# Kernel tuning notes

Hardware: AMD Instinct MI355X
Metric: run time of the kernel (lower is better)

Reference implementation:

```python
import jax, jax.numpy as jnp
import numpy as np

D_MODEL = 1024
NUM_HEADS = 16
HEAD_DIM = D_MODEL // NUM_HEADS
D_FF = 4096
BATCH = 4
SEQ = 2048
LN_EPS = 1e-6
NEG_INF = -1e10


def setup_inputs() -> dict:
    key = jax.random.key(0)
    ks = jax.random.split(key, 8)
    def lin_init(k, fan_in, fan_out):
        # flax default: lecun_normal kernel, zeros bias
        w = jax.random.normal(k, (fan_in, fan_out), jnp.float32) / np.sqrt(fan_in)
        b = jnp.zeros((fan_out,), jnp.float32)
        return w, b
    x = jax.random.normal(ks[0], (BATCH, SEQ, D_MODEL), jnp.float32)
    w_qkv, b_qkv = lin_init(ks[1], D_MODEL, 3 * D_MODEL)
    w_out, b_out = lin_init(ks[2], D_MODEL, D_MODEL)
    w_fc1, b_fc1 = lin_init(ks[3], D_MODEL, D_FF)
    w_fc2, b_fc2 = lin_init(ks[4], D_FF, D_MODEL)
    ln1_scale = jnp.ones((D_MODEL,), jnp.float32)
    ln1_bias = jnp.zeros((D_MODEL,), jnp.float32)
    ln2_scale = jnp.ones((D_MODEL,), jnp.float32)
    ln2_bias = jnp.zeros((D_MODEL,), jnp.float32)
    return {
        'x': x,
        'w_qkv': w_qkv, 'b_qkv': b_qkv,
        'w_out': w_out, 'b_out': b_out,
        'w_fc1': w_fc1, 'b_fc1': b_fc1,
        'w_fc2': w_fc2, 'b_fc2': b_fc2,
        'ln1_scale': ln1_scale, 'ln1_bias': ln1_bias,
        'ln2_scale': ln2_scale, 'ln2_bias': ln2_bias,
    }


def _layernorm(x, scale, bias):
    mu = jnp.mean(x, axis=-1, keepdims=True)
    var = jnp.mean(jnp.square(x - mu), axis=-1, keepdims=True)
    return (x - mu) * jax.lax.rsqrt(var + LN_EPS) * scale + bias


def _attention(x, w_qkv, b_qkv, w_out, b_out):
    B, S, _ = x.shape
    qkv = x @ w_qkv + b_qkv                      # [B,S,3*D]
    qkv = qkv.reshape(B, S, 3, NUM_HEADS, HEAD_DIM)
    q, k, v = qkv[:, :, 0], qkv[:, :, 1], qkv[:, :, 2]   # [B,S,H,D]
    q = q.transpose(0, 2, 1, 3)                  # [B,H,S,D]
    k = k.transpose(0, 2, 1, 3)
    v = v.transpose(0, 2, 1, 3)
    scores = jnp.einsum('bhqd,bhkd->bhqk', q, k) / np.sqrt(HEAD_DIM)
    causal = jnp.tril(jnp.ones((S, S), bool))[None, None]
    scores = jnp.where(causal, scores, NEG_INF)
    attn = jax.nn.softmax(scores, axis=-1)
    out = jnp.einsum('bhqk,bhkd->bhqd', attn, v)  # [B,H,S,D]
    out = out.transpose(0, 2, 1, 3).reshape(B, S, D_MODEL)
    return out @ w_out + b_out


def _mlp(x, w_fc1, b_fc1, w_fc2, b_fc2):
    h = jax.nn.gelu(x @ w_fc1 + b_fc1)  # approximate (tanh) gelu, matching nnx.gelu default
    return h @ w_fc2 + b_fc2


def reference(x, w_qkv, b_qkv, w_out, b_out, w_fc1, b_fc1, w_fc2, b_fc2,
              ln1_scale, ln1_bias, ln2_scale, ln2_bias):
    x = x + _attention(_layernorm(x, ln1_scale, ln1_bias), w_qkv, b_qkv, w_out, b_out)
    x = x + _mlp(_layernorm(x, ln2_scale, ln2_bias), w_fc1, b_fc1, w_fc2, b_fc2)
    return x
```

## Files before the change

kernel.cpp:

```cpp
#include <hip/hip_runtime.h>

typedef unsigned short u16;
typedef unsigned int u32;
typedef __bf16 bf16x8 __attribute__((ext_vector_type(8)));
typedef float f32x4 __attribute__((ext_vector_type(4)));

constexpr int SEQ = 2048;

__device__ __forceinline__ float bf2f(u16 u) {
    u32 x = ((u32)u) << 16;
    return __builtin_bit_cast(float, x);
}
__device__ __forceinline__ u16 f2bf(float f) {
    u32 u = __builtin_bit_cast(u32, f);
    u32 r = u + 0x7fffu + ((u >> 16) & 1u);
    return (u16)(r >> 16);
}
__device__ __forceinline__ u32 cvt_pk_bf16(float a, float b) {
    u32 d;
    asm("v_cvt_pk_bf16_f32 %0, %1, %2" : "=v"(d) : "v"(a), "v"(b));
    return d;
}
__device__ __forceinline__ bf16x8 ld_frag(const u16* p) {
    uint4 u = *(const uint4*)p;
    return __builtin_bit_cast(bf16x8, u);
}
__device__ __forceinline__ float gelu_f(float x) {
    float u = 0.7978845608028654f * (x + 0.044715f * x * x * x);
    float e = exp2f(u * 2.885390081777927f);
    float t = 1.f - 2.f / (1.f + e);
    return 0.5f * x * (1.f + t);
}
__device__ __forceinline__ bool probe_f32(const u32* p) { return (p[0] & 0xFFFFu) == 0u; }

__device__ __forceinline__ void load_lds16(const u16* g, u16* l) {
    __builtin_amdgcn_global_load_lds(
        (const __attribute__((address_space(1))) void*)g,
        (__attribute__((address_space(3))) void*)l, 16, 0, 0);
}

__device__ __forceinline__ void xcd_map(int& bx, int& by) {
    const int gx = gridDim.x;
    const int n = gx * gridDim.y;
    const int orig = blockIdx.y * gx + blockIdx.x;
    const int id = (orig & 7) * (n >> 3) + (orig >> 3);
    bx = id % gx;
    by = id / gx;
}

__global__ __launch_bounds__(256) void convert_to_bf16(const void* __restrict__ in, long long off,
                                                       u16* __restrict__ out, int n,
                                                       const u32* __restrict__ probe) {
    const bool f32 = probe_f32(probe);
    int i = (blockIdx.x * 256 + threadIdx.x) * 4;
    if (i >= n) return;
    if (f32) {
        const float4 v = *(const float4*)((const float*)in + off + i);
        uint2 o;
        o.x = (u32)f2bf(v.x) | ((u32)f2bf(v.y) << 16);
        o.y = (u32)f2bf(v.z) | ((u32)f2bf(v.w) << 16);
        *(uint2*)(out + i) = o;
    } else {
        *(uint2*)(out + i) = *(const uint2*)((const u16*)in + off + i);
    }
}

__global__ __launch_bounds__(256) void transpose_any(const void* __restrict__ in,
                                                     u16* __restrict__ out,
                                                     int K, int N, const u32* __restrict__ probe) {
    const bool f32 = probe_f32(probe);
    __shared__ u16 tile[32][33];
    int tx = threadIdx.x & 31, ty = threadIdx.x >> 5;
    int k0 = blockIdx.y * 32, n0 = blockIdx.x * 32;
    for (int i = 0; i < 32; i += 8) {
        size_t idx = (size_t)(k0 + ty + i) * N + n0 + tx;
        tile[ty + i][tx] = f32 ? f2bf(((const float*)in)[idx]) : ((const u16*)in)[idx];
    }
    __syncthreads();
    for (int i = 0; i < 32; i += 8)
        out[(size_t)(n0 + ty + i) * K + k0 + tx] = tile[tx][ty + i];
}

__global__ __launch_bounds__(256) void fused_cvt_ln(const void* __restrict__ xraw, long long off,
                                                    const u16* __restrict__ sc,
                                                    const u16* __restrict__ bi,
                                                    u16* __restrict__ xbf,
                                                    u16* __restrict__ xn,
                                                    const u32* __restrict__ probe) {
    const bool f32 = probe_f32(probe);
    int row = blockIdx.x;
    int tid = threadIdx.x;
    float v[4];
    if (f32) {
        const float4 q = *(const float4*)((const float*)xraw + off + (size_t)row * 1024 + tid * 4);
        v[0] = q.x; v[1] = q.y; v[2] = q.z; v[3] = q.w;
    } else {
        uint2 u = *(const uint2*)((const u16*)xraw + off + (size_t)row * 1024 + tid * 4);
        v[0] = bf2f((u16)(u.x & 0xffffu)); v[1] = bf2f((u16)(u.x >> 16));
        v[2] = bf2f((u16)(u.y & 0xffffu)); v[3] = bf2f((u16)(u.y >> 16));
    }
    {
        uint2 c;
        c.x = (u32)f2bf(v[0]) | ((u32)f2bf(v[1]) << 16);
        c.y = (u32)f2bf(v[2]) | ((u32)f2bf(v[3]) << 16);
        *(uint2*)(xbf + (size_t)row * 1024 + tid * 4) = c;
    }
    float s1 = 0.f, s2 = 0.f;
    for (int i = 0; i < 4; i++) { s1 += v[i]; s2 += v[i] * v[i]; }
    for (int off2 = 32; off2 >= 1; off2 >>= 1) {
        s1 += __shfl_xor(s1, off2, 64);
        s2 += __shfl_xor(s2, off2, 64);
    }
    __shared__ float red[8];
    int wave = tid >> 6, lane = tid & 63;
    if (lane == 0) { red[wave] = s1; red[4 + wave] = s2; }
    __syncthreads();
    s1 = red[0] + red[1] + red[2] + red[3];
    s2 = red[4] + red[5] + red[6] + red[7];
    float mean = s1 * (1.f / 1024.f);
    float var = s2 * (1.f / 1024.f) - mean * mean;
    float rstd = rsqrtf(var + 1e-6f);
    int c = tid * 4;
    float y0 = (v[0] - mean) * rstd * bf2f(sc[c + 0]) + bf2f(bi[c + 0]);
    float y1 = (v[1] - mean) * rstd * bf2f(sc[c + 1]) + bf2f(bi[c + 1]);
    float y2 = (v[2] - mean) * rstd * bf2f(sc[c + 2]) + bf2f(bi[c + 2]);
    float y3 = (v[3] - mean) * rstd * bf2f(sc[c + 3]) + bf2f(bi[c + 3]);
    uint2 ov;
    ov.x = (u32)f2bf(y0) | ((u32)f2bf(y1) << 16);
    ov.y = (u32)f2bf(y2) | ((u32)f2bf(y3) << 16);
    *(uint2*)(xn + (size_t)row * 1024 + tid * 4) = ov;
}

__global__ __launch_bounds__(256) void layernorm_k(const u16* __restrict__ x,
                                                   const u16* __restrict__ sc,
                                                   const u16* __restrict__ bi,
                                                   u16* __restrict__ out) {
    int row = blockIdx.x;
    int tid = threadIdx.x;
    const u16* xr = x + (size_t)row * 1024;
    uint2 u = *(const uint2*)(xr + tid * 4);
    float v[4];
    v[0] = bf2f((u16)(u.x & 0xffffu));
    v[1] = bf2f((u16)(u.x >> 16));
    v[2] = bf2f((u16)(u.y & 0xffffu));
    v[3] = bf2f((u16)(u.y >> 16));
    float s1 = 0.f, s2 = 0.f;
    for (int i = 0; i < 4; i++) { s1 += v[i]; s2 += v[i] * v[i]; }
    for (int off = 32; off >= 1; off >>= 1) {
        s1 += __shfl_xor(s1, off, 64);
        s2 += __shfl_xor(s2, off, 64);
    }
    __shared__ float red[8];
    int wave = tid >> 6, lane = tid & 63;
    if (lane == 0) { red[wave] = s1; red[4 + wave] = s2; }
    __syncthreads();
    s1 = red[0] + red[1] + red[2] + red[3];
    s2 = red[4] + red[5] + red[6] + red[7];
    float mean = s1 * (1.f / 1024.f);
    float var = s2 * (1.f / 1024.f) - mean * mean;
    float rstd = rsqrtf(var + 1e-6f);
    u32 o0, o1;
    {
        int c = tid * 4;
        float y0 = (v[0] - mean) * rstd * bf2f(sc[c + 0]) + bf2f(bi[c + 0]);
        float y1 = (v[1] - mean) * rstd * bf2f(sc[c + 1]) + bf2f(bi[c + 1]);
        float y2 = (v[2] - mean) * rstd * bf2f(sc[c + 2]) + bf2f(bi[c + 2]);
        float y3 = (v[3] - mean) * rstd * bf2f(sc[c + 3]) + bf2f(bi[c + 3]);
        o0 = (u32)f2bf(y0) | ((u32)f2bf(y1) << 16);
        o1 = (u32)f2bf(y2) | ((u32)f2bf(y3) << 16);
    }
    uint2 ov; ov.x = o0; ov.y = o1;
    *(uint2*)(out + (size_t)row * 1024 + tid * 4) = ov;
}

__device__ __forceinline__ void gemm_core(const u16* __restrict__ A, const u16* __restrict__ Bt,
                                          int K, int bm, int bn,
                                          u16* lA, u16* lB, f32x4 acc[4][4]) {
    const int tid = threadIdx.x, lane = tid & 63, wave = tid >> 6;
    const int wr = (wave >> 1) * 64, wc = (wave & 1) * 64;
    const int g = lane >> 4, l15 = lane & 15;
    const int srow = wave * 32 + (lane >> 3);
    const int gslot = (lane & 7) ^ (lane >> 3);
    const u16* gA = A + (size_t)(bm + srow) * K + gslot * 8;
    const u16* gB = Bt + (size_t)(bn + srow) * K + gslot * 8;
    const int sw = (l15 & 7);
    const int nt = K >> 6;

    {
        u16* dA = lA + wave * 2048;
        u16* dB = lB + wave * 2048;
#pragma unroll
        for (int q = 0; q < 4; q++) {
            load_lds16(gA + q * 8 * K, dA + q * 512);
            load_lds16(gB + q * 8 * K, dB + q * 512);
        }
    }

    for (int t = 0; t < nt; t++) {
        const int cur = (t & 1) * 8192;
        __syncthreads();
        if (t + 1 < nt) {
            const int nxt = ((t + 1) & 1) * 8192;
            const int kk = (t + 1) * 64;
            u16* dA = lA + nxt + wave * 2048;
            u16* dB = lB + nxt + wave * 2048;
#pragma unroll
            for (int q = 0; q < 4; q++) {
                load_lds16(gA + kk + q * 8 * K, dA + q * 512);
                load_lds16(gB + kk + q * 8 * K, dB + q * 512);
            }
        }
        const u16* cA = lA + cur;
        const u16* cB = lB + cur;
#pragma unroll
        for (int kh = 0; kh < 2; kh++) {
            bf16x8 af[4], bfr[4];
#pragma unroll
            for (int i = 0; i < 4; i++)
                af[i] = ld_frag(cA + (wr + i * 16 + l15) * 64 + (((kh * 4 + g) ^ sw) * 8));
#pragma unroll
            for (int j = 0; j < 4; j++)
                bfr[j] = ld_frag(cB + (wc + j * 16 + l15) * 64 + (((kh * 4 + g) ^ sw) * 8));
#pragma unroll
            for (int i = 0; i < 4; i++)
#pragma unroll
                for (int j = 0; j < 4; j++)
                    acc[i][j] = __builtin_amdgcn_mfma_f32_16x16x32_bf16(bfr[j], af[i], acc[i][j], 0, 0, 0);
        }
    }
}

__global__ __launch_bounds__(256) void gemm_bt(const u16* __restrict__ A,
                                               const u16* __restrict__ Bt,
                                               const u16* __restrict__ bias,
                                               const u16* __restrict__ res,
                                               void* __restrict__ out,
                                               int M, int N, int K, int epi,
                                               long long ooff, const u32* __restrict__ probe) {
    __shared__ __align__(16) u16 lA[2 * 128 * 64];
    __shared__ __align__(16) u16 lB[2 * 128 * 64];
    const int tid = threadIdx.x, lane = tid & 63, wave = tid >> 6;
    const int wr = (wave >> 1) * 64, wc = (wave & 1) * 64;
    const int g = lane >> 4, l15 = lane & 15;
    int bxi, byi;
    xcd_map(bxi, byi);
    const int bm = byi * 128, bn = bxi * 128;

    f32x4 acc[4][4];
    f32x4 zero = {0.f, 0.f, 0.f, 0.f};
    for (int i = 0; i < 4; i++)
        for (int j = 0; j < 4; j++) acc[i][j] = zero;

    gemm_core(A, Bt, K, bm, bn, lA, lB, acc);

    const bool of32 = (epi == 3) && probe_f32(probe);
    for (int j = 0; j < 4; j++) {
        const int gn0 = bn + wc + j * 16 + g * 4;
        const uint2 bv2 = *(const uint2*)(bias + gn0);
        const float b0 = bf2f((u16)(bv2.x & 0xffffu)), b1 = bf2f((u16)(bv2.x >> 16));
        const float b2 = bf2f((u16)(bv2.y & 0xffffu)), b3 = bf2f((u16)(bv2.y >> 16));
        for (int i = 0; i < 4; i++) {
            const int gm = bm + wr + i * 16 + l15;
            float v0 = acc[i][j][0] + b0, v1 = acc[i][j][1] + b1;
            float v2 = acc[i][j][2] + b2, v3 = acc[i][j][3] + b3;
            if (epi == 1 || epi == 3) {
                const uint2 rv = *(const uint2*)(res + (size_t)gm * N + gn0);
                v0 += bf2f((u16)(rv.x & 0xffffu)); v1 += bf2f((u16)(rv.x >> 16));
                v2 += bf2f((u16)(rv.y & 0xffffu)); v3 += bf2f((u16)(rv.y >> 16));
            } else if (epi == 2) {
                v0 = gelu_f(v0); v1 = gelu_f(v1); v2 = gelu_f(v2); v3 = gelu_f(v3);
            }
            if (epi == 3) {
                if (of32) {
                    float4 o = {v0, v1, v2, v3};
                    *(float4*)((float*)out + ooff + (size_t)gm * N + gn0) = o;
                } else {
                    uint2 o;
                    o.x = cvt_pk_bf16(v0, v1); o.y = cvt_pk_bf16(v2, v3);
                    *(uint2*)((u16*)out + ooff + (size_t)gm * N + gn0) = o;
                }
            } else {
                uint2 o;
                o.x = cvt_pk_bf16(v0, v1); o.y = cvt_pk_bf16(v2, v3);
                *(uint2*)((u16*)out + (size_t)gm * N + gn0) = o;
            }
        }
    }
}

__global__ __launch_bounds__(256) void gemm_qkv(const u16* __restrict__ A,
                                                const u16* __restrict__ Bt,
                                                const u16* __restrict__ bias,
                                                u16* __restrict__ Qg,
                                                u16* __restrict__ Kg,
                                                u16* __restrict__ VTg,
                                                int K) {
    __shared__ __align__(16) u16 lA[2 * 128 * 64];
    __shared__ __align__(16) u16 lB[2 * 128 * 64];
    const int tid = threadIdx.x, lane = tid & 63, wave = tid >> 6;
    const int wr = (wave >> 1) * 64, wc = (wave & 1) * 64;
    const int g = lane >> 4, l15 = lane & 15;
    int bxi, byi;
    xcd_map(bxi, byi);
    const int bm = byi * 128, bn = bxi * 128;
    const float QSCALE = 0.18033688011112042f;

    f32x4 acc[4][4];
    f32x4 zero = {0.f, 0.f, 0.f, 0.f};
    for (int i = 0; i < 4; i++)
        for (int j = 0; j < 4; j++) acc[i][j] = zero;

    gemm_core(A, Bt, K, bm, bn, lA, lB, acc);

    for (int j = 0; j < 4; j++) {
        const int gn0 = bn + wc + j * 16 + g * 4;
        const int which = gn0 >> 10;
        const int hh = (gn0 >> 6) & 15, d0 = gn0 & 63;
        const uint2 bv2 = *(const uint2*)(bias + gn0);
        const float b0 = bf2f((u16)(bv2.x & 0xffffu)), b1 = bf2f((u16)(bv2.x >> 16));
        const float b2 = bf2f((u16)(bv2.y & 0xffffu)), b3 = bf2f((u16)(bv2.y >> 16));
        for (int i = 0; i < 4; i++) {
            const int s0 = bm + wr + i * 16 + l15;
            const int b = s0 >> 11, srel = s0 & 2047;
            const int bh = b * 16 + hh;
            const float v0 = acc[i][j][0] + b0, v1 = acc[i][j][1] + b1;
            const float v2 = acc[i][j][2] + b2, v3 = acc[i][j][3] + b3;
            if (which == 0) {
                uint2 o;
                o.x = cvt_pk_bf16(v0 * QSCALE, v1 * QSCALE);
                o.y = cvt_pk_bf16(v2 * QSCALE, v3 * QSCALE);
                *(uint2*)(Qg + ((size_t)bh * SEQ + srel) * 64 + d0) = o;
            } else if (which == 1) {
                uint2 o;
                o.x = cvt_pk_bf16(v0, v1); o.y = cvt_pk_bf16(v2, v3);
                *(uint2*)(Kg + ((size_t)bh * SEQ + srel) * 64 + d0) = o;
            } else {
                VTg[((size_t)bh * 64 + d0 + 0) * SEQ + srel] = f2bf(v0);
                VTg[((size_t)bh * 64 + d0 + 1) * SEQ + srel] = f2bf(v1);
                VTg[((size_t)bh * 64 + d0 + 2) * SEQ + srel] = f2bf(v2);
                VTg[((size_t)bh * 64 + d0 + 3) * SEQ + srel] = f2bf(v3);
            }
        }
    }
}

__device__ __forceinline__ void stage_kv(const u16* Kbh, const u16* Vbh, int kv0,
                                         u16* bK, u16* bV, int lane, int wave) {
    const int r = lane >> 3;
    const int gs = ((lane & 7) ^ r) * 8;
#pragma unroll
    for (int q = 0; q < 2; q++) {
        const int row = q * 32 + wave * 8 + r;
        load_lds16(Kbh + (size_t)(kv0 + row) * 64 + gs, bK + q * 2048 + wave * 512 + lane * 8);
        load_lds16(Vbh + (size_t)row * SEQ + kv0 + gs, bV + q * 2048 + wave * 512 + lane * 8);
    }
}

__global__ __launch_bounds__(256) void flash_attn6(const u16* __restrict__ Qg,
                                                   const u16* __restrict__ Kg,
                                                   const u16* __restrict__ VTg,
                                                   u16* __restrict__ attn) {
    __shared__ __align__(16) u16 lK[2][64 * 64];
    __shared__ __align__(16) u16 lVt[2][64 * 64];
    __shared__ __align__(16) u16 lP[4 * 32 * 72];

    int bxi, byi;
    xcd_map(bxi, byi);
    const int bh = byi;
    const int tid = threadIdx.x, lane = tid & 63, wave = tid >> 6;
    const int g = lane >> 4, l15 = lane & 15;
    const float MASKV = -3.0e4f;

    const u16* Qbh = Qg + (size_t)bh * SEQ * 64;
    const u16* Kbh = Kg + (size_t)bh * SEQ * 64;
    const u16* Vbh = VTg + (size_t)bh * 64 * SEQ;
    u16* myP = lP + wave * 32 * 72;
    const int b = bh >> 4, h = bh & 15;
    const f32x4 zero = {0.f, 0.f, 0.f, 0.f};
    const int sw = (l15 & 7);

    for (int ph = 0; ph < 2; ph++) {
        const int ti = ph ? bxi : (15 - bxi);
        const int q0 = ti * 128;
        const int qw = q0 + wave * 32;
        const int nfull = q0 >> 6;
        const int nt = nfull + 2;

        bf16x8 qf[2][2];
#pragma unroll
        for (int mi = 0; mi < 2; mi++)
#pragma unroll
            for (int kh = 0; kh < 2; kh++)
                qf[mi][kh] = ld_frag(Qbh + (size_t)(qw + mi * 16 + l15) * 64 + kh * 32 + g * 8);

        float l_[2] = {0.f, 0.f};
        f32x4 o[2][4];
        for (int mi = 0; mi < 2; mi++)
            for (int nj = 0; nj < 4; nj++) o[mi][nj] = zero;

        __syncthreads();
        stage_kv(Kbh, Vbh, 0, lK[0], lVt[0], lane, wave);

        for (int t = 0; t < nt; t++) {
            __syncthreads();
            if (t + 1 < nt)
                stage_kv(Kbh, Vbh, (t + 1) * 64, lK[(t + 1) & 1], lVt[(t + 1) & 1], lane, wave);
            const u16* bK = lK[t & 1];
            const u16* bV = lVt[t & 1];
            const bool diag = (t >= nfull);
            const int kv0 = t * 64;

            f32x4 sc[4][2];
#pragma unroll
            for (int ki = 0; ki < 4; ki++)
                for (int mi = 0; mi < 2; mi++) sc[ki][mi] = zero;
#pragma unroll
            for (int kh = 0; kh < 2; kh++) {
                bf16x8 kf[4];
#pragma unroll
                for (int ki = 0; ki < 4; ki++)
                    kf[ki] = ld_frag(bK + (ki * 16 + l15) * 64 + (((kh * 4 + g) ^ sw) * 8));
#pragma unroll
                for (int ki = 0; ki < 4; ki++)
#pragma unroll
                    for (int mi = 0; mi < 2; mi++)
                        sc[ki][mi] = __builtin_amdgcn_mfma_f32_16x16x32_bf16(kf[ki], qf[mi][kh], sc[ki][mi], 0, 0, 0);
            }

#pragma unroll
            for (int mi = 0; mi < 2; mi++) {
                const int qrow = qw + mi * 16 + l15;
                u16* pr = myP + (mi * 16 + l15) * 72 + g * 4;
                float lacc = 0.f;
#pragma unroll
                for (int ki = 0; ki < 4; ki++) {
                    const int kvb = kv0 + ki * 16 + g * 4;
                    float v0 = sc[ki][mi][0], v1 = sc[ki][mi][1];
                    float v2 = sc[ki][mi][2], v3 = sc[ki][mi][3];
                    if (diag) {
                        if (kvb + 0 > qrow) v0 = MASKV;
                        if (kvb + 1 > qrow) v1 = MASKV;
                        if (kvb + 2 > qrow) v2 = MASKV;
                        if (kvb + 3 > qrow) v3 = MASKV;
                    }
                    const float e0 = exp2f(v0), e1 = exp2f(v1);
                    const float e2 = exp2f(v2), e3 = exp2f(v3);
                    lacc += (e0 + e1) + (e2 + e3);
                    uint2 pw;
                    pw.x = cvt_pk_bf16(e0, e1);
                    pw.y = cvt_pk_bf16(e2, e3);
                    *(uint2*)(pr + ki * 16) = pw;
                }
                l_[mi] += lacc;
            }

#pragma unroll
            for (int ks = 0; ks < 2; ks++) {
                bf16x8 pa[2], vb[4];
#pragma unroll
                for (int mi = 0; mi < 2; mi++)
                    pa[mi] = ld_frag(myP + (mi * 16 + l15) * 72 + ks * 32 + g * 8);
#pragma unroll
                for (int nj = 0; nj < 4; nj++)
                    vb[nj] = ld_frag(bV + (nj * 16 + l15) * 64 + (((ks * 4 + g) ^ sw) * 8));
#pragma unroll
                for (int mi = 0; mi < 2; mi++)
#pragma unroll
                    for (int nj = 0; nj < 4; nj++)
                        o[mi][nj] = __builtin_amdgcn_mfma_f32_16x16x32_bf16(pa[mi], vb[nj], o[mi][nj], 0, 0, 0);
            }
        }

#pragma unroll
        for (int mi = 0; mi < 2; mi++) {
            float ls = l_[mi];
            ls += __shfl_xor(ls, 16, 64);
            ls += __shfl_xor(ls, 32, 64);
#pragma unroll
            for (int r = 0; r < 4; r++) {
                const float inv = 1.f / __shfl(ls, g * 4 + r, 64);
                const int row = qw + mi * 16 + g * 4 + r;
                const size_t orow = ((size_t)b * SEQ + row) * 1024 + h * 64;
                for (int nj = 0; nj < 4; nj++)
                    attn[orow + nj * 16 + l15] = f2bf(o[mi][nj][r] * inv);
            }
        }
    }
}

extern "C" void kernel_launch(void* const* d_in, const int* in_sizes, int n_in,
                              void* d_out, int out_size, void* d_ws, size_t ws_size,
                              hipStream_t stream) {
    const u32* probe = (const u32*)d_in[9];
    char* ws = (char*)d_ws;
    const size_t MB = 1048576;
    auto T = [&](size_t mb) { return (u16*)(ws + mb * MB); };
    auto conv = [&](const void* src, long long off, u16* dst, int n) {
        convert_to_bf16<<<(n / 4 + 255) / 256, 256, 0, stream>>>(src, off, dst, n, probe);
    };

    if (ws_size >= 160 * MB) {
        u16* xn1 = T(0), *Qg = T(16), *Kg = T(32), *VTg = T(48), *hbuf = T(0);
        u16* attn = T(64), *xn2 = T(64), *xbf = T(80), *resid1 = T(96);
        u16* wTq = T(128), *wTo = T(134), *wT1 = T(136), *wT2 = T(144), *vecs = T(152);
        u16 *bqkvC = vecs, *boutC = vecs + 3072, *bfc1C = vecs + 4096, *bfc2C = vecs + 8192;
        u16 *ln1sC = vecs + 9216, *ln1bC = vecs + 10240, *ln2sC = vecs + 11264, *ln2bC = vecs + 12288;
        conv(d_in[2], 0, bqkvC, 3072); conv(d_in[4], 0, boutC, 1024);
        conv(d_in[6], 0, bfc1C, 4096); conv(d_in[8], 0, bfc2C, 1024);
        conv(d_in[9], 0, ln1sC, 1024); conv(d_in[10], 0, ln1bC, 1024);
        conv(d_in[11], 0, ln2sC, 1024); conv(d_in[12], 0, ln2bC, 1024);
        transpose_any<<<dim3(96, 32), 256, 0, stream>>>(d_in[1], wTq, 1024, 3072, probe);
        transpose_any<<<dim3(32, 32), 256, 0, stream>>>(d_in[3], wTo, 1024, 1024, probe);
        transpose_any<<<dim3(128, 32), 256, 0, stream>>>(d_in[5], wT1, 1024, 4096, probe);
        transpose_any<<<dim3(32, 128), 256, 0, stream>>>(d_in[7], wT2, 4096, 1024, probe);
        fused_cvt_ln<<<8192, 256, 0, stream>>>(d_in[0], 0, ln1sC, ln1bC, xbf, xn1, probe);
        gemm_qkv<<<dim3(24, 64), 256, 0, stream>>>(xn1, wTq, bqkvC, Qg, Kg, VTg, 1024);
        flash_attn6<<<dim3(8, 64), 256, 0, stream>>>(Qg, Kg, VTg, attn);
        gemm_bt<<<dim3(8, 64), 256, 0, stream>>>(attn, wTo, boutC, xbf, resid1, 8192, 1024, 1024, 1, 0, probe);
        layernorm_k<<<8192, 256, 0, stream>>>(resid1, ln2sC, ln2bC, xn2);
        gemm_bt<<<dim3(32, 64), 256, 0, stream>>>(xn2, wT1, bfc1C, nullptr, hbuf, 8192, 4096, 1024, 2, 0, probe);
        gemm_bt<<<dim3(8, 64), 256, 0, stream>>>(hbuf, wT2, bfc2C, resid1, d_out, 8192, 1024, 4096, 3, 0, probe);
    } else {
        u16* vecs = T(0);
        u16 *bqkvC = vecs, *boutC = vecs + 3072, *bfc1C = vecs + 4096, *bfc2C = vecs + 8192;
        u16 *ln1sC = vecs + 9216, *ln1bC = vecs + 10240, *ln2sC = vecs + 11264, *ln2bC = vecs + 12288;
        u16* wTq = T(1), *wTo = T(7), *wT1 = T(9), *wT2 = T(17);
        u16* xbf = T(25), *xn = T(29), *Qg = T(33), *Kg = T(37), *VTg = T(41);
        u16* attn_b = T(45), *resid_b = T(49), *h_b = T(53);
        conv(d_in[2], 0, bqkvC, 3072); conv(d_in[4], 0, boutC, 1024);
        conv(d_in[6], 0, bfc1C, 4096); conv(d_in[8], 0, bfc2C, 1024);
        conv(d_in[9], 0, ln1sC, 1024); conv(d_in[10], 0, ln1bC, 1024);
        conv(d_in[11], 0, ln2sC, 1024); conv(d_in[12], 0, ln2bC, 1024);
        transpose_any<<<dim3(96, 32), 256, 0, stream>>>(d_in[1], wTq, 1024, 3072, probe);
        transpose_any<<<dim3(32, 32), 256, 0, stream>>>(d_in[3], wTo, 1024, 1024, probe);
        transpose_any<<<dim3(128, 32), 256, 0, stream>>>(d_in[5], wT1, 1024, 4096, probe);
        transpose_any<<<dim3(32, 128), 256, 0, stream>>>(d_in[7], wT2, 4096, 1024, probe);
        for (int b = 0; b < 4; b++) {
            const long long ro = (long long)b * 2048 * 1024;
            fused_cvt_ln<<<2048, 256, 0, stream>>>(d_in[0], ro, ln1sC, ln1bC, xbf, xn, probe);
            gemm_qkv<<<dim3(24, 16), 256, 0, stream>>>(xn, wTq, bqkvC, Qg, Kg, VTg, 1024);
            flash_attn6<<<dim3(8, 16), 256, 0, stream>>>(Qg, Kg, VTg, attn_b);
            gemm_bt<<<dim3(8, 16), 256, 0, stream>>>(attn_b, wTo, boutC, xbf, resid_b, 2048, 1024, 1024, 1, 0, probe);
            layernorm_k<<<2048, 256, 0, stream>>>(resid_b, ln2sC, ln2bC, xn);
            for (int c = 0; c < 2; c++) {
                u16* xnc = xn + (size_t)c * 1024 * 1024;
                u16* resc = resid_b + (size_t)c * 1024 * 1024;
                gemm_bt<<<dim3(32, 8), 256, 0, stream>>>(xnc, wT1, bfc1C, nullptr, h_b, 1024, 4096, 1024, 2, 0, probe);
                gemm_bt<<<dim3(8, 8), 256, 0, stream>>>(h_b, wT2, bfc2C, resc, d_out, 1024, 1024, 4096, 3, ro + (long long)c * 1048576, probe);
            }
        }
    }
}
```

Measured before the change: 539.5 us.

## Replace double-buffered GEMM LDS pipeline with single buffer and optional XCD remap

The shared GEMM core drops its double-buffered LDS prefetch in favour of a single 128x64 buffer per operand, with a barrier before and after each tile load. This halves LDS use per block, which may allow more resident blocks per CU, but it removes the overlap of global loads with MFMA work. A remap flag also disables the XCD block remapping for the FC1 GEMM while keeping it for the other GEMMs.

```diff
diff --git a/kernel.cpp b/kernel.cpp
--- a/kernel.cpp
+++ b/kernel.cpp
@@ -183,44 +183,27 @@
     const int gslot = (lane & 7) ^ (lane >> 3);
     const u16* gA = A + (size_t)(bm + srow) * K + gslot * 8;
     const u16* gB = Bt + (size_t)(bn + srow) * K + gslot * 8;
+    u16* lAb = lA + wave * 2048;
+    u16* lBb = lB + wave * 2048;
     const int sw = (l15 & 7);
-    const int nt = K >> 6;
-
-    {
-        u16* dA = lA + wave * 2048;
-        u16* dB = lB + wave * 2048;
+
+    for (int kk = 0; kk < K; kk += 64) {
+        __syncthreads();
 #pragma unroll
         for (int q = 0; q < 4; q++) {
-            load_lds16(gA + q * 8 * K, dA + q * 512);
-            load_lds16(gB + q * 8 * K, dB + q * 512);
-        }
-    }
-
-    for (int t = 0; t < nt; t++) {
-        const int cur = (t & 1) * 8192;
+            load_lds16(gA + kk + q * 8 * K, lAb + q * 512);
+            load_lds16(gB + kk + q * 8 * K, lBb + q * 512);
+        }
         __syncthreads();
-        if (t + 1 < nt) {
-            const int nxt = ((t + 1) & 1) * 8192;
-            const int kk = (t + 1) * 64;
-            u16* dA = lA + nxt + wave * 2048;
-            u16* dB = lB + nxt + wave * 2048;
-#pragma unroll
-            for (int q = 0; q < 4; q++) {
-                load_lds16(gA + kk + q * 8 * K, dA + q * 512);
-                load_lds16(gB + kk + q * 8 * K, dB + q * 512);
-            }
-        }
-        const u16* cA = lA + cur;
-        const u16* cB = lB + cur;
 #pragma unroll
         for (int kh = 0; kh < 2; kh++) {
             bf16x8 af[4], bfr[4];
 #pragma unroll
             for (int i = 0; i < 4; i++)
-                af[i] = ld_frag(cA + (wr + i * 16 + l15) * 64 + (((kh * 4 + g) ^ sw) * 8));
+                af[i] = ld_frag(lA + (wr + i * 16 + l15) * 64 + (((kh * 4 + g) ^ sw) * 8));
 #pragma unroll
             for (int j = 0; j < 4; j++)
-                bfr[j] = ld_frag(cB + (wc + j * 16 + l15) * 64 + (((kh * 4 + g) ^ sw) * 8));
+                bfr[j] = ld_frag(lB + (wc + j * 16 + l15) * 64 + (((kh * 4 + g) ^ sw) * 8));
 #pragma unroll
             for (int i = 0; i < 4; i++)
 #pragma unroll
@@ -236,14 +219,15 @@
                                                const u16* __restrict__ res,
                                                void* __restrict__ out,
                                                int M, int N, int K, int epi,
-                                               long long ooff, const u32* __restrict__ probe) {
-    __shared__ __align__(16) u16 lA[2 * 128 * 64];
-    __shared__ __align__(16) u16 lB[2 * 128 * 64];
+                                               long long ooff, const u32* __restrict__ probe,
+                                               int remap) {
+    __shared__ __align__(16) u16 lA[128 * 64];
+    __shared__ __align__(16) u16 lB[128 * 64];
     const int tid = threadIdx.x, lane = tid & 63, wave = tid >> 6;
     const int wr = (wave >> 1) * 64, wc = (wave & 1) * 64;
     const int g = lane >> 4, l15 = lane & 15;
-    int bxi, byi;
-    xcd_map(bxi, byi);
+    int bxi = blockIdx.x, byi = blockIdx.y;
+    if (remap) xcd_map(bxi, byi);
     const int bm = byi * 128, bn = bxi * 128;
 
     f32x4 acc[4][4];
@@ -295,8 +279,8 @@
                                                 u16* __restrict__ Kg,
                                                 u16* __restrict__ VTg,
                                                 int K) {
-    __shared__ __align__(16) u16 lA[2 * 128 * 64];
-    __shared__ __align__(16) u16 lB[2 * 128 * 64];
+    __shared__ __align__(16) u16 lA[128 * 64];
+    __shared__ __align__(16) u16 lB[128 * 64];
     const int tid = threadIdx.x, lane = tid & 63, wave = tid >> 6;
     const int wr = (wave >> 1) * 64, wc = (wave & 1) * 64;
     const int g = lane >> 4, l15 = lane & 15;
@@ -516,10 +500,10 @@
         fused_cvt_ln<<<8192, 256, 0, stream>>>(d_in[0], 0, ln1sC, ln1bC, xbf, xn1, probe);
         gemm_qkv<<<dim3(24, 64), 256, 0, stream>>>(xn1, wTq, bqkvC, Qg, Kg, VTg, 1024);
         flash_attn6<<<dim3(8, 64), 256, 0, stream>>>(Qg, Kg, VTg, attn);
-        gemm_bt<<<dim3(8, 64), 256, 0, stream>>>(attn, wTo, boutC, xbf, resid1, 8192, 1024, 1024, 1, 0, probe);
+        gemm_bt<<<dim3(8, 64), 256, 0, stream>>>(attn, wTo, boutC, xbf, resid1, 8192, 1024, 1024, 1, 0, probe, 1);
         layernorm_k<<<8192, 256, 0, stream>>>(resid1, ln2sC, ln2bC, xn2);
-        gemm_bt<<<dim3(32, 64), 256, 0, stream>>>(xn2, wT1, bfc1C, nullptr, hbuf, 8192, 4096, 1024, 2, 0, probe);
-        gemm_bt<<<dim3(8, 64), 256, 0, stream>>>(hbuf, wT2, bfc2C, resid1, d_out, 8192, 1024, 4096, 3, 0, probe);
+        gemm_bt<<<dim3(32, 64), 256, 0, stream>>>(xn2, wT1, bfc1C, nullptr, hbuf, 8192, 4096, 1024, 2, 0, probe, 0);
+        gemm_bt<<<dim3(8, 64), 256, 0, stream>>>(hbuf, wT2, bfc2C, resid1, d_out, 8192, 1024, 4096, 3, 0, probe, 1);
     } else {
         u16* vecs = T(0);
         u16 *bqkvC = vecs, *boutC = vecs + 3072, *bfc1C = vecs + 4096, *bfc2C = vecs + 8192;
@@ -540,14 +524,14 @@
             fused_cvt_ln<<<2048, 256, 0, stream>>>(d_in[0], ro, ln1sC, ln1bC, xbf, xn, probe);
             gemm_qkv<<<dim3(24, 16), 256, 0, stream>>>(xn, wTq, bqkvC, Qg, Kg, VTg, 1024);
             flash_attn6<<<dim3(8, 16), 256, 0, stream>>>(Qg, Kg, VTg, attn_b);
-            gemm_bt<<<dim3(8, 16), 256, 0, stream>>>(attn_b, wTo, boutC, xbf, resid_b, 2048, 1024, 1024, 1, 0, probe);
+            gemm_bt<<<dim3(8, 16), 256, 0, stream>>>(attn_b, wTo, boutC, xbf, resid_b, 2048, 1024, 1024, 1, 0, probe, 1);
             layernorm_k<<<2048, 256, 0, stream>>>(resid_b, ln2sC, ln2bC, xn);
             for (int c = 0; c < 2; c++) {
                 u16* xnc = xn + (size_t)c * 1024 * 1024;
                 u16* resc = resid_b + (size_t)c * 1024 * 1024;
-                gemm_bt<<<dim3(32, 8), 256, 0, stream>>>(xnc, wT1, bfc1C, nullptr, h_b, 1024, 4096, 1024, 2, 0, probe);
-                gemm_bt<<<dim3(8, 8), 256, 0, stream>>>(h_b, wT2, bfc2C, resc, d_out, 1024, 1024, 4096, 3, ro + (long long)c * 1048576, probe);
-            }
-        }
-    }
-}
+                gemm_bt<<<dim3(32, 8), 256, 0, stream>>>(xnc, wT1, bfc1C, nullptr, h_b, 1024, 4096, 1024, 2, 0, probe, 0);
+                gemm_bt<<<dim3(8, 8), 256, 0, stream>>>(h_b, wT2, bfc2C, resc, d_out, 1024, 1024, 4096, 3, ro + (long long)c * 1048576, probe, 1);
+            }
+        }
+    }
+}
```

New measurement: 568.4 us. 1.05x slower.
